# Kernel optimization log

Measured on AMD Instinct MI355X. Metric: run time of the kernel, lower is better.

The kernel has to match this reference:

```python
import jax, jax.numpy as jnp
import numpy as np

N_NODES = 100000


def setup_inputs() -> dict:
    key = jax.random.key(0)
    ks = jax.random.split(key, 6)
    x = jax.random.normal(ks[0], (N_NODES, 3), dtype=jnp.float32)
    edge_index = jax.random.randint(ks[1], (2, 1600000), 0, N_NODES, dtype=jnp.int32)
    W1 = jax.random.normal(ks[2], (6, 64), dtype=jnp.float32) * 0.2
    b1 = jnp.zeros((64,), dtype=jnp.float32)
    W2 = jax.random.normal(ks[3], (67, 128), dtype=jnp.float32) * 0.1
    b2 = jnp.zeros((128,), dtype=jnp.float32)
    Wc = jax.random.normal(ks[4], (128, 5), dtype=jnp.float32) * 0.1
    bc = jnp.zeros((5,), dtype=jnp.float32)
    return {"x": x, "edge_index": edge_index, "W1": W1, "b1": b1,
            "W2": W2, "b2": b2, "Wc": Wc, "bc": bc}


def _pointnet_conv(h, rel, src, dst, W, b, n):
    # gather neighbor features, MLP on [h_j, pos_j - pos_i], max-aggregate per node
    msg = jnp.concatenate([h[src], rel], axis=-1) @ W + b  # [E, out]
    agg = jax.ops.segment_max(msg, dst, num_segments=n)    # [N, out]
    return jax.nn.relu(agg)  # relu also maps -inf (isolated nodes) to 0


def reference(x, edge_index, W1, b1, W2, b2, Wc, bc):
    src, dst = edge_index[0], edge_index[1]
    pos = x  # forward uses data.x for both x and pos
    rel = pos[src] - pos[dst]                       # [E, 3]
    h = _pointnet_conv(x, rel, src, dst, W1, b1, N_NODES)   # [N, 64]
    h = _pointnet_conv(h, rel, src, dst, W2, b2, N_NODES)   # [N, 128]
    logits = h @ Wc + bc                            # [N, 5]
    return jax.nn.log_softmax(logits, axis=-1)
```

## Files before the change

kernel.cpp:

```cpp
#include <hip/hip_runtime.h>
#include <cstdint>

#define CAP 56
#define NBITS 8
#define BINSZ 256
#define BIN_CAP 5120
#define TILE_E 4096
#define MAXBINS 512

typedef _Float16 h2 __attribute__((ext_vector_type(2)));
typedef _Float16 h4 __attribute__((ext_vector_type(4)));

static __device__ inline h4 pkmax4(h4 a, h4 b) {
#if __has_builtin(__builtin_elementwise_max)
    return __builtin_elementwise_max(a, b);
#else
    h4 r;
    h2 alo = {a.x,a.y}, ahi = {a.z,a.w}, blo = {b.x,b.y}, bhi = {b.z,b.w}, rlo, rhi;
    asm("v_pk_max_f16 %0, %1, %2" : "=v"(rlo) : "v"(alo), "v"(blo));
    asm("v_pk_max_f16 %0, %1, %2" : "=v"(rhi) : "v"(ahi), "v"(bhi));
    r.x=rlo.x; r.y=rlo.y; r.z=rhi.x; r.w=rhi.y;
    return r;
#endif
}

__global__ __launch_bounds__(256) void bin_kernel(
    const int* __restrict__ ei, int* __restrict__ bin_cnt,
    int* __restrict__ pairs, int E, int nbins)
{
    __shared__ int hist[MAXBINS];
    __shared__ int base[MAXBINS];
    __shared__ int lofs[MAXBINS];
    int t = threadIdx.x;
    for (int i = t; i < nbins; i += 256) hist[i] = 0;
    __syncthreads();
    int e0 = blockIdx.x * TILE_E;
    int s[16], d[16];
    #pragma unroll
    for (int i = 0; i < 16; ++i) {
        int e = e0 + t + i * 256;
        bool ok = e < E;
        s[i] = ok ? ei[e] : 0;
        d[i] = ok ? ei[E + e] : -1;
        if (ok) atomicAdd(&hist[d[i] >> NBITS], 1);
    }
    __syncthreads();
    for (int i = t; i < nbins; i += 256) {
        base[i] = atomicAdd(&bin_cnt[i], hist[i]);
        lofs[i] = 0;
    }
    __syncthreads();
    #pragma unroll
    for (int i = 0; i < 16; ++i) {
        if (d[i] >= 0) {
            int b = d[i] >> NBITS;
            int p = base[b] + atomicAdd(&lofs[b], 1);
            if (p < BIN_CAP)
                pairs[b * BIN_CAP + p] = s[i] | ((d[i] & (BINSZ - 1)) << 17);
        }
    }
}

__global__ __launch_bounds__(256) void scatter2_kernel(
    const int* __restrict__ pairs, const int* __restrict__ bin_cnt,
    int* __restrict__ cursor, int* __restrict__ bucket, int N)
{
    __shared__ int cur[BINSZ];
    __shared__ int lbuck[BINSZ * CAP];
    int t = threadIdx.x;
    int b = blockIdx.x;
    for (int i = t; i < BINSZ; i += 256) cur[i] = 0;
    __syncthreads();
    int cnt = min(bin_cnt[b], BIN_CAP);
    const int* pp = pairs + b * BIN_CAP;
    for (int i = t; i < cnt; i += 256) {
        int w = pp[i];
        int p = atomicAdd(&cur[w >> 17], 1);
        if (p < CAP) lbuck[(w >> 17) * CAP + p] = w & 0x1FFFF;
    }
    __syncthreads();
    int nbase = b * BINSZ;
    for (int dl = t; dl < BINSZ; dl += 256) {
        int n = nbase + dl;
        if (n >= N) continue;
        int c = min(cur[dl], CAP);
        int e = (c + 7) & ~7;
        int s0 = (c > 0) ? lbuck[dl * CAP] : 0;
        for (int p = c; p < e; ++p) lbuck[dl * CAP + p] = s0;
        cursor[n] = c;
    }
    __syncthreads();
    int4* dst = (int4*)(bucket + (size_t)nbase * CAP);
    const int4* srcv = (const int4*)lbuck;
    for (int i = t; i < BINSZ * CAP / 4; i += 256) dst[i] = srcv[i];
}

__global__ __launch_bounds__(256) void v1_kernel(
    const float* __restrict__ x, const float* __restrict__ W1,
    const float* __restrict__ b1, h2* __restrict__ v1h, int N)
{
    int tid = blockIdx.x * 256 + threadIdx.x;
    int n = tid >> 5, f = tid & 31;
    if (n >= N) return;
    float2 q0 = ((const float2*)(W1 + 0*64))[f];
    float2 q1 = ((const float2*)(W1 + 1*64))[f];
    float2 q2 = ((const float2*)(W1 + 2*64))[f];
    float2 t0 = ((const float2*)(W1 + 3*64))[f];
    float2 t1 = ((const float2*)(W1 + 4*64))[f];
    float2 t2 = ((const float2*)(W1 + 5*64))[f];
    float2 bb = ((const float2*)b1)[f];
    float x0 = x[n*3], x1 = x[n*3+1], x2 = x[n*3+2];
    h2 o;
    o.x = (_Float16)(bb.x + x0*(q0.x+t0.x) + x1*(q1.x+t1.x) + x2*(q2.x+t2.x));
    o.y = (_Float16)(bb.y + x0*(q0.y+t0.y) + x1*(q1.y+t1.y) + x2*(q2.y+t2.y));
    v1h[tid] = o;
}

__global__ __launch_bounds__(256) void agg1_kernel(
    const float* __restrict__ x, const int* __restrict__ cursor,
    const int* __restrict__ bucket, const float* __restrict__ W1,
    const h4* __restrict__ v1v, float* __restrict__ h1, int N)
{
    int gid = blockIdx.x * 256 + threadIdx.x;
    int n   = gid >> 4;
    int sub = threadIdx.x & 15;
    if (n >= N) return;
    int cnt = min(cursor[n], CAP);
    int rounds = (cnt + 7) & ~7;
    const int* brow = bucket + (size_t)n * CAP;
    const _Float16 NEG = (_Float16)(-60000.0f);
    h4 hm = { NEG, NEG, NEG, NEG };
    for (int j0 = 0; j0 < rounds; j0 += 8) {
        h4 vv[8];
        #pragma unroll
        for (int u = 0; u < 8; ++u)
            vv[u] = v1v[(size_t)brow[j0+u] * 16 + sub];
        #pragma unroll
        for (int u = 0; u < 8; ++u) hm = pkmax4(hm, vv[u]);
    }
    float4 t0 = ((const float4*)(W1 + 3*64))[sub];
    float4 t1 = ((const float4*)(W1 + 4*64))[sub];
    float4 t2 = ((const float4*)(W1 + 5*64))[sub];
    float x0 = x[n*3], x1 = x[n*3+1], x2 = x[n*3+2];
    float4 o;
    o.x = (cnt > 0) ? fmaxf((float)hm.x - (x0*t0.x + x1*t1.x + x2*t2.x), 0.f) : 0.f;
    o.y = (cnt > 0) ? fmaxf((float)hm.y - (x0*t0.y + x1*t1.y + x2*t2.y), 0.f) : 0.f;
    o.z = (cnt > 0) ? fmaxf((float)hm.z - (x0*t0.z + x1*t1.z + x2*t2.z), 0.f) : 0.f;
    o.w = (cnt > 0) ? fmaxf((float)hm.w - (x0*t0.w + x1*t1.w + x2*t2.w), 0.f) : 0.f;
    ((float4*)h1)[(size_t)n * 16 + sub] = o;
}

__global__ __launch_bounds__(256) void gemm_u2_kernel(
    const float* __restrict__ x, const float* __restrict__ h1,
    const float* __restrict__ W2, const float* __restrict__ b2,
    h4* __restrict__ u2h, int N)
{
    __shared__ float h1T[64][72];
    int tid = threadIdx.x;
    int n0  = blockIdx.x * 64;
    {
        int r = tid >> 2, kc = (tid & 3) * 16;
        const float4* src = (const float4*)(h1 + (size_t)(n0 + r) * 64 + kc);
        bool ok = (n0 + r) < N;
        #pragma unroll
        for (int i = 0; i < 4; ++i) {
            float4 v = ok ? src[i] : make_float4(0.f,0.f,0.f,0.f);
            h1T[kc + 4*i + 0][r] = v.x;
            h1T[kc + 4*i + 1][r] = v.y;
            h1T[kc + 4*i + 2][r] = v.z;
            h1T[kc + 4*i + 3][r] = v.w;
        }
    }
    __syncthreads();
    int fi = tid & 31;
    int ni = tid >> 5;
    float acc[8][4];
    #pragma unroll
    for (int r = 0; r < 8; ++r)
        #pragma unroll
        for (int c = 0; c < 4; ++c) acc[r][c] = 0.f;

    const float4* W2v = (const float4*)W2;
    #pragma unroll 4
    for (int k = 0; k < 64; ++k) {
        float4 w  = W2v[k*32 + fi];
        float4 a0 = *(const float4*)&h1T[k][ni*8];
        float4 a1 = *(const float4*)&h1T[k][ni*8+4];
        float hv[8] = {a0.x,a0.y,a0.z,a0.w,a1.x,a1.y,a1.z,a1.w};
        #pragma unroll
        for (int r = 0; r < 8; ++r) {
            acc[r][0] = fmaf(hv[r], w.x, acc[r][0]);
            acc[r][1] = fmaf(hv[r], w.y, acc[r][1]);
            acc[r][2] = fmaf(hv[r], w.z, acc[r][2]);
            acc[r][3] = fmaf(hv[r], w.w, acc[r][3]);
        }
    }
    float4 bb = ((const float4*)b2)[fi];
    float4 wa = W2v[64*32 + fi], wb = W2v[65*32 + fi], wc = W2v[66*32 + fi];
    #pragma unroll
    for (int r = 0; r < 8; ++r) {
        int n = n0 + ni*8 + r;
        if (n >= N) break;
        float x0 = x[n*3], x1 = x[n*3+1], x2 = x[n*3+2];
        h4 o4;
        o4.x = (_Float16)(acc[r][0] + bb.x + x0*wa.x + x1*wb.x + x2*wc.x);
        o4.y = (_Float16)(acc[r][1] + bb.y + x0*wa.y + x1*wb.y + x2*wc.y);
        o4.z = (_Float16)(acc[r][2] + bb.z + x0*wa.z + x1*wb.z + x2*wc.z);
        o4.w = (_Float16)(acc[r][3] + bb.w + x0*wa.w + x1*wb.w + x2*wc.w);
        u2h[(size_t)n * 32 + fi] = o4;
    }
}

__global__ __launch_bounds__(256) void agg2_head_kernel(
    const float* __restrict__ x, const int* __restrict__ cursor,
    const int* __restrict__ bucket, const float* __restrict__ W2,
    const h4* __restrict__ u2v, const float* __restrict__ Wc,
    const float* __restrict__ bc, float* __restrict__ out, int N)
{
    int gid = blockIdx.x * 256 + threadIdx.x;
    int n   = gid >> 5;
    int sub = threadIdx.x & 31;
    if (n >= N) return;
    int cnt = min(cursor[n], CAP);
    int rounds = (cnt + 7) & ~7;
    const int* brow = bucket + (size_t)n * CAP;
    const _Float16 NEG = (_Float16)(-60000.0f);
    h4 hm = { NEG, NEG, NEG, NEG };
    for (int j0 = 0; j0 < rounds; j0 += 8) {
        h4 vv[8];
        #pragma unroll
        for (int u = 0; u < 8; ++u)
            vv[u] = u2v[(size_t)brow[j0+u] * 32 + sub];
        #pragma unroll
        for (int u = 0; u < 8; ++u) hm = pkmax4(hm, vv[u]);
    }
    float4 wa = ((const float4*)(W2 + 64*128))[sub];
    float4 wb = ((const float4*)(W2 + 65*128))[sub];
    float4 wc = ((const float4*)(W2 + 66*128))[sub];
    float x0 = x[n*3], x1 = x[n*3+1], x2 = x[n*3+2];
    float hh0 = (cnt > 0) ? fmaxf((float)hm.x - (x0*wa.x + x1*wb.x + x2*wc.x), 0.f) : 0.f;
    float hh1 = (cnt > 0) ? fmaxf((float)hm.y - (x0*wa.y + x1*wb.y + x2*wc.y), 0.f) : 0.f;
    float hh2 = (cnt > 0) ? fmaxf((float)hm.z - (x0*wa.z + x1*wb.z + x2*wc.z), 0.f) : 0.f;
    float hh3 = (cnt > 0) ? fmaxf((float)hm.w - (x0*wa.w + x1*wb.w + x2*wc.w), 0.f) : 0.f;

    int g = sub * 4;
    float l0 = hh0*Wc[g*5+0] + hh1*Wc[(g+1)*5+0] + hh2*Wc[(g+2)*5+0] + hh3*Wc[(g+3)*5+0];
    float l1 = hh0*Wc[g*5+1] + hh1*Wc[(g+1)*5+1] + hh2*Wc[(g+2)*5+1] + hh3*Wc[(g+3)*5+1];
    float l2 = hh0*Wc[g*5+2] + hh1*Wc[(g+1)*5+2] + hh2*Wc[(g+2)*5+2] + hh3*Wc[(g+3)*5+2];
    float l3 = hh0*Wc[g*5+3] + hh1*Wc[(g+1)*5+3] + hh2*Wc[(g+2)*5+3] + hh3*Wc[(g+3)*5+3];
    float l4 = hh0*Wc[g*5+4] + hh1*Wc[(g+1)*5+4] + hh2*Wc[(g+2)*5+4] + hh3*Wc[(g+3)*5+4];
    #pragma unroll
    for (int off = 16; off > 0; off >>= 1) {
        l0 += __shfl_xor(l0, off);
        l1 += __shfl_xor(l1, off);
        l2 += __shfl_xor(l2, off);
        l3 += __shfl_xor(l3, off);
        l4 += __shfl_xor(l4, off);
    }
    l0 += bc[0]; l1 += bc[1]; l2 += bc[2]; l3 += bc[3]; l4 += bc[4];
    float mx  = fmaxf(fmaxf(fmaxf(l0, l1), fmaxf(l2, l3)), l4);
    float s   = expf(l0-mx) + expf(l1-mx) + expf(l2-mx) + expf(l3-mx) + expf(l4-mx);
    float lse = mx + logf(s);
    if (sub < 5) {
        float v = (sub == 0) ? l0 : (sub == 1) ? l1 : (sub == 2) ? l2
                : (sub == 3) ? l3 : l4;
        out[n*5 + sub] = v - lse;
    }
}

extern "C" void kernel_launch(void* const* d_in, const int* in_sizes, int n_in,
                              void* d_out, int out_size, void* d_ws, size_t ws_size,
                              hipStream_t stream)
{
    const float* x  = (const float*)d_in[0];
    const int*   ei = (const int*)d_in[1];
    const float* W1 = (const float*)d_in[2];
    const float* b1 = (const float*)d_in[3];
    const float* W2 = (const float*)d_in[4];
    const float* b2 = (const float*)d_in[5];
    const float* Wc = (const float*)d_in[6];
    const float* bc = (const float*)d_in[7];
    float* out = (float*)d_out;

    int N = in_sizes[0] / 3;
    int E = in_sizes[1] / 2;
    int nbins = (N + BINSZ - 1) / BINSZ;

    char* ws = (char*)d_ws;
    h4*    u2h     = (h4*)   (ws);
    h2*    v1h     = (h2*)   (ws + 25600000);
    int*   pairs   = (int*)  (ws + 38400000);
    float* h1      = (float*)(ws + 46500000);
    int*   bucket  = (int*)  (ws + 72100000);
    int*   cursor  = (int*)  (ws + 94600000);
    int*   bin_cnt = (int*)  (ws + 95000000);

    (void)hipMemsetAsync(bin_cnt, 0, 2048, stream);

    bin_kernel<<<(E + TILE_E - 1) / TILE_E, 256, 0, stream>>>(
        ei, bin_cnt, pairs, E, nbins);
    scatter2_kernel<<<nbins, 256, 0, stream>>>(pairs, bin_cnt, cursor, bucket, N);

    v1_kernel<<<(N * 32 + 255) / 256, 256, 0, stream>>>(x, W1, b1, v1h, N);
    agg1_kernel<<<(N * 16 + 255) / 256, 256, 0, stream>>>(
        x, cursor, bucket, W1, (const h4*)v1h, h1, N);
    gemm_u2_kernel<<<(N + 63) / 64, 256, 0, stream>>>(x, h1, W2, b2, u2h, N);
    agg2_head_kernel<<<(N * 32 + 255) / 256, 256, 0, stream>>>(
        x, cursor, bucket, W2, u2h, Wc, bc, out, N);
}
```

Before: 256.3 us.

## Stage bin writes through shared memory and recompute layer-1 messages from packed positions

```diff
diff --git a/kernel.cpp b/kernel.cpp
--- a/kernel.cpp
+++ b/kernel.cpp
@@ -6,7 +6,7 @@
 #define BINSZ 256
 #define BIN_CAP 5120
 #define TILE_E 4096
-#define MAXBINS 512
+#define SCANN 512
 
 typedef _Float16 h2 __attribute__((ext_vector_type(2)));
 typedef _Float16 h4 __attribute__((ext_vector_type(4)));
@@ -28,11 +28,13 @@
     const int* __restrict__ ei, int* __restrict__ bin_cnt,
     int* __restrict__ pairs, int E, int nbins)
 {
-    __shared__ int hist[MAXBINS];
-    __shared__ int base[MAXBINS];
-    __shared__ int lofs[MAXBINS];
+    __shared__ int hist[SCANN];
+    __shared__ int sc[SCANN];
+    __shared__ int gbase[SCANN];
+    __shared__ int lofs[SCANN];
+    __shared__ int words[TILE_E];
     int t = threadIdx.x;
-    for (int i = t; i < nbins; i += 256) hist[i] = 0;
+    for (int i = t; i < SCANN; i += 256) { hist[i] = 0; lofs[i] = 0; }
     __syncthreads();
     int e0 = blockIdx.x * TILE_E;
     int s[16], d[16];
@@ -45,19 +47,35 @@
         if (ok) atomicAdd(&hist[d[i] >> NBITS], 1);
     }
     __syncthreads();
-    for (int i = t; i < nbins; i += 256) {
-        base[i] = atomicAdd(&bin_cnt[i], hist[i]);
-        lofs[i] = 0;
-    }
+    sc[t] = hist[t]; sc[t + 256] = hist[t + 256];
+    __syncthreads();
+    for (int off = 1; off < SCANN; off <<= 1) {
+        int i0 = t, i1 = t + 256;
+        int v0 = (i0 >= off) ? sc[i0 - off] : 0;
+        int v1 = (i1 >= off) ? sc[i1 - off] : 0;
+        __syncthreads();
+        sc[i0] += v0; sc[i1] += v1;
+        __syncthreads();
+    }
+    for (int i = t; i < nbins; i += 256)
+        gbase[i] = atomicAdd(&bin_cnt[i], hist[i]);
     __syncthreads();
     #pragma unroll
     for (int i = 0; i < 16; ++i) {
         if (d[i] >= 0) {
             int b = d[i] >> NBITS;
-            int p = base[b] + atomicAdd(&lofs[b], 1);
-            if (p < BIN_CAP)
-                pairs[b * BIN_CAP + p] = s[i] | ((d[i] & (BINSZ - 1)) << 17);
+            int p = atomicAdd(&lofs[b], 1);
+            words[(sc[b] - hist[b]) + p] = s[i] | ((d[i] & (BINSZ - 1)) << 17);
         }
+    }
+    __syncthreads();
+    int total = sc[nbins - 1];
+    for (int i = t; i < total; i += 256) {
+        int lo = 0, hi = nbins - 1;
+        while (lo < hi) { int mid = (lo + hi) >> 1; if (sc[mid] > i) hi = mid; else lo = mid + 1; }
+        int b = lo;
+        int off = gbase[b] + (i - (sc[b] - hist[b]));
+        if (off < BIN_CAP) pairs[b * BIN_CAP + off] = words[i];
     }
 }
 
@@ -95,58 +113,61 @@
     for (int i = t; i < BINSZ * CAP / 4; i += 256) dst[i] = srcv[i];
 }
 
-__global__ __launch_bounds__(256) void v1_kernel(
-    const float* __restrict__ x, const float* __restrict__ W1,
-    const float* __restrict__ b1, h2* __restrict__ v1h, int N)
-{
-    int tid = blockIdx.x * 256 + threadIdx.x;
-    int n = tid >> 5, f = tid & 31;
-    if (n >= N) return;
-    float2 q0 = ((const float2*)(W1 + 0*64))[f];
-    float2 q1 = ((const float2*)(W1 + 1*64))[f];
-    float2 q2 = ((const float2*)(W1 + 2*64))[f];
-    float2 t0 = ((const float2*)(W1 + 3*64))[f];
-    float2 t1 = ((const float2*)(W1 + 4*64))[f];
-    float2 t2 = ((const float2*)(W1 + 5*64))[f];
-    float2 bb = ((const float2*)b1)[f];
-    float x0 = x[n*3], x1 = x[n*3+1], x2 = x[n*3+2];
-    h2 o;
-    o.x = (_Float16)(bb.x + x0*(q0.x+t0.x) + x1*(q1.x+t1.x) + x2*(q2.x+t2.x));
-    o.y = (_Float16)(bb.y + x0*(q0.y+t0.y) + x1*(q1.y+t1.y) + x2*(q2.y+t2.y));
-    v1h[tid] = o;
+__global__ __launch_bounds__(256) void xpack_kernel(
+    const float* __restrict__ x, float4* __restrict__ xp, int N)
+{
+    int n = blockIdx.x * 256 + threadIdx.x;
+    if (n < N) xp[n] = make_float4(x[n*3], x[n*3+1], x[n*3+2], 0.f);
 }
 
 __global__ __launch_bounds__(256) void agg1_kernel(
-    const float* __restrict__ x, const int* __restrict__ cursor,
+    const float4* __restrict__ xp, const int* __restrict__ cursor,
     const int* __restrict__ bucket, const float* __restrict__ W1,
-    const h4* __restrict__ v1v, float* __restrict__ h1, int N)
+    const float* __restrict__ b1, float* __restrict__ h1, int N)
 {
     int gid = blockIdx.x * 256 + threadIdx.x;
     int n   = gid >> 4;
     int sub = threadIdx.x & 15;
     if (n >= N) return;
+    float4 q0 = ((const float4*)(W1 + 0*64))[sub];
+    float4 q1 = ((const float4*)(W1 + 1*64))[sub];
+    float4 q2 = ((const float4*)(W1 + 2*64))[sub];
+    float4 t0 = ((const float4*)(W1 + 3*64))[sub];
+    float4 t1 = ((const float4*)(W1 + 4*64))[sub];
+    float4 t2 = ((const float4*)(W1 + 5*64))[sub];
+    float4 c0 = make_float4(q0.x+t0.x, q0.y+t0.y, q0.z+t0.z, q0.w+t0.w);
+    float4 c1 = make_float4(q1.x+t1.x, q1.y+t1.y, q1.z+t1.z, q1.w+t1.w);
+    float4 c2 = make_float4(q2.x+t2.x, q2.y+t2.y, q2.z+t2.z, q2.w+t2.w);
+
     int cnt = min(cursor[n], CAP);
     int rounds = (cnt + 7) & ~7;
     const int* brow = bucket + (size_t)n * CAP;
-    const _Float16 NEG = (_Float16)(-60000.0f);
-    h4 hm = { NEG, NEG, NEG, NEG };
+    float4 m = make_float4(-3e38f, -3e38f, -3e38f, -3e38f);
     for (int j0 = 0; j0 < rounds; j0 += 8) {
-        h4 vv[8];
-        #pragma unroll
-        for (int u = 0; u < 8; ++u)
-            vv[u] = v1v[(size_t)brow[j0+u] * 16 + sub];
-        #pragma unroll
-        for (int u = 0; u < 8; ++u) hm = pkmax4(hm, vv[u]);
-    }
-    float4 t0 = ((const float4*)(W1 + 3*64))[sub];
-    float4 t1 = ((const float4*)(W1 + 4*64))[sub];
-    float4 t2 = ((const float4*)(W1 + 5*64))[sub];
-    float x0 = x[n*3], x1 = x[n*3+1], x2 = x[n*3+2];
+        int sj[8];
+        #pragma unroll
+        for (int u = 0; u < 8; ++u) sj[u] = brow[j0 + u];
+        float4 xs[8];
+        #pragma unroll
+        for (int u = 0; u < 8; ++u) xs[u] = xp[sj[u]];
+        #pragma unroll
+        for (int u = 0; u < 8; ++u) {
+            float4 v;
+            v.x = fmaf(xs[u].x, c0.x, fmaf(xs[u].y, c1.x, xs[u].z * c2.x));
+            v.y = fmaf(xs[u].x, c0.y, fmaf(xs[u].y, c1.y, xs[u].z * c2.y));
+            v.z = fmaf(xs[u].x, c0.z, fmaf(xs[u].y, c1.z, xs[u].z * c2.z));
+            v.w = fmaf(xs[u].x, c0.w, fmaf(xs[u].y, c1.w, xs[u].z * c2.w));
+            m.x = fmaxf(m.x, v.x); m.y = fmaxf(m.y, v.y);
+            m.z = fmaxf(m.z, v.z); m.w = fmaxf(m.w, v.w);
+        }
+    }
+    float4 bb = ((const float4*)b1)[sub];
+    float4 xd = xp[n];
     float4 o;
-    o.x = (cnt > 0) ? fmaxf((float)hm.x - (x0*t0.x + x1*t1.x + x2*t2.x), 0.f) : 0.f;
-    o.y = (cnt > 0) ? fmaxf((float)hm.y - (x0*t0.y + x1*t1.y + x2*t2.y), 0.f) : 0.f;
-    o.z = (cnt > 0) ? fmaxf((float)hm.z - (x0*t0.z + x1*t1.z + x2*t2.z), 0.f) : 0.f;
-    o.w = (cnt > 0) ? fmaxf((float)hm.w - (x0*t0.w + x1*t1.w + x2*t2.w), 0.f) : 0.f;
+    o.x = (cnt > 0) ? fmaxf(m.x + bb.x - (xd.x*t0.x + xd.y*t1.x + xd.z*t2.x), 0.f) : 0.f;
+    o.y = (cnt > 0) ? fmaxf(m.y + bb.y - (xd.x*t0.y + xd.y*t1.y + xd.z*t2.y), 0.f) : 0.f;
+    o.z = (cnt > 0) ? fmaxf(m.z + bb.z - (xd.x*t0.z + xd.y*t1.z + xd.z*t2.z), 0.f) : 0.f;
+    o.w = (cnt > 0) ? fmaxf(m.w + bb.w - (xd.x*t0.w + xd.y*t1.w + xd.z*t2.w), 0.f) : 0.f;
     ((float4*)h1)[(size_t)n * 16 + sub] = o;
 }
 
@@ -287,23 +308,23 @@
     int nbins = (N + BINSZ - 1) / BINSZ;
 
     char* ws = (char*)d_ws;
-    h4*    u2h     = (h4*)   (ws);
-    h2*    v1h     = (h2*)   (ws + 25600000);
-    int*   pairs   = (int*)  (ws + 38400000);
-    float* h1      = (float*)(ws + 46500000);
-    int*   bucket  = (int*)  (ws + 72100000);
-    int*   cursor  = (int*)  (ws + 94600000);
-    int*   bin_cnt = (int*)  (ws + 95000000);
+    h4*     u2h     = (h4*)    (ws);
+    float4* xp      = (float4*)(ws + 25600000);
+    int*    pairs   = (int*)   (ws + 27200000);
+    float*  h1      = (float*) (ws + 35250000);
+    int*    bucket  = (int*)   (ws + 60850000);
+    int*    cursor  = (int*)   (ws + 83300000);
+    int*    bin_cnt = (int*)   (ws + 83700000);
 
     (void)hipMemsetAsync(bin_cnt, 0, 2048, stream);
 
+    xpack_kernel<<<(N + 255) / 256, 256, 0, stream>>>(x, xp, N);
     bin_kernel<<<(E + TILE_E - 1) / TILE_E, 256, 0, stream>>>(
         ei, bin_cnt, pairs, E, nbins);
     scatter2_kernel<<<nbins, 256, 0, stream>>>(pairs, bin_cnt, cursor, bucket, N);
 
-    v1_kernel<<<(N * 32 + 255) / 256, 256, 0, stream>>>(x, W1, b1, v1h, N);
     agg1_kernel<<<(N * 16 + 255) / 256, 256, 0, stream>>>(
-        x, cursor, bucket, W1, (const h4*)v1h, h1, N);
+        xp, cursor, bucket, W1, b1, h1, N);
     gemm_u2_kernel<<<(N + 63) / 64, 256, 0, stream>>>(x, h1, W2, b2, u2h, N);
     agg2_head_kernel<<<(N * 32 + 255) / 256, 256, 0, stream>>>(
         x, cursor, bucket, W2, u2h, Wc, bc, out, N);
```

Result: faster. 248.2 us (-3.2%).
